# Kernel optimization log

Measured on AMD Instinct MI355X. Metric: run time of the kernel, lower is better.

Reference implementation:

```python
import jax, jax.numpy as jnp
import numpy as np

NEG_SLOPE = 0.2  # PyG GATConv default negative_slope


def gat_conv(x, src, dst, W, a_src, a_dst, b, concat):
    """One PyG-style GATConv (eval mode, self-loops already added to src/dst).
    x: [N, Fin], W: [Fin, H*C], a_src/a_dst: [H, C], b: [H*C] or [C].
    """
    N = x.shape[0]
    H, C = a_src.shape
    h = (x @ W).reshape(N, H, C)                       # [N,H,C]
    alpha_s = jnp.sum(h * a_src, axis=-1)              # [N,H]
    alpha_d = jnp.sum(h * a_dst, axis=-1)              # [N,H]
    e = alpha_s[src] + alpha_d[dst]                    # [E,H]
    e = jax.nn.leaky_relu(e, NEG_SLOPE)
    # scatter-softmax over incoming edges of each destination node
    m = jax.ops.segment_max(e, dst, num_segments=N)    # [N,H]
    p = jnp.exp(e - m[dst])                            # [E,H]
    s = jax.ops.segment_sum(p, dst, num_segments=N)    # [N,H]
    alpha = p / s[dst]                                 # [E,H]
    msg = h[src] * alpha[:, :, None]                   # [E,H,C]
    out = jax.ops.segment_sum(msg, dst, num_segments=N)  # [N,H,C]
    out = out.reshape(N, H * C) if concat else out.mean(axis=1)
    return out + b


def setup_inputs() -> dict:
    key = jax.random.key(0)
    ks = jax.random.split(key, 12)
    N, E = 50000, 800000
    IN_C, HID, HEADS, OUT_C = 1, 32, 4, 1
    HW = HID * HEADS  # 128
    x = jax.random.normal(ks[0], (N, IN_C), dtype=jnp.float32)
    edge_index = jax.random.randint(ks[1], (2, E), 0, N, dtype=jnp.int64)
    g = 0.1
    inp = {
        "x": x,
        "edge_index": edge_index,
        "W1": jax.random.normal(ks[2], (IN_C, HW), dtype=jnp.float32) * g,
        "a_src1": jax.random.normal(ks[3], (HEADS, HID), dtype=jnp.float32) * g,
        "a_dst1": jax.random.normal(ks[4], (HEADS, HID), dtype=jnp.float32) * g,
        "b1": jnp.zeros((HW,), dtype=jnp.float32),
        "W2": jax.random.normal(ks[5], (HW, HW), dtype=jnp.float32) * g,
        "a_src2": jax.random.normal(ks[6], (HEADS, HID), dtype=jnp.float32) * g,
        "a_dst2": jax.random.normal(ks[7], (HEADS, HID), dtype=jnp.float32) * g,
        "b2": jnp.zeros((HW,), dtype=jnp.float32),
        "W3": jax.random.normal(ks[8], (HW, OUT_C), dtype=jnp.float32) * g,
        "a_src3": jax.random.normal(ks[9], (1, OUT_C), dtype=jnp.float32) * g,
        "a_dst3": jax.random.normal(ks[10], (1, OUT_C), dtype=jnp.float32) * g,
        "b3": jnp.zeros((OUT_C,), dtype=jnp.float32),
    }
    return inp


def reference(x, edge_index, W1, a_src1, a_dst1, b1, W2, a_src2, a_dst2, b2,
              W3, a_src3, a_dst3, b3):
    N = x.shape[0]
    loop = jnp.arange(N, dtype=edge_index.dtype)
    # PyG GATConv add_self_loops=True (each layer): add once, reused by all layers
    src = jnp.concatenate([edge_index[0], loop])
    dst = jnp.concatenate([edge_index[1], loop])
    h = gat_conv(x, src, dst, W1, a_src1, a_dst1, b1, concat=True)
    h = jax.nn.elu(h)  # dropout is identity in eval mode
    h = gat_conv(h, src, dst, W2, a_src2, a_dst2, b2, concat=True)
    h = jax.nn.elu(h)
    out = gat_conv(h, src, dst, W3, a_src3, a_dst3, b3, concat=False)
    return out
```

## Files before the change

kernel.cpp:

```cpp
#include <hip/hip_runtime.h>
#include <math.h>

#define NEG_SLOPE 0.2f
#define MAXDEG 64

typedef _Float16 hv4 __attribute__((ext_vector_type(4)));
typedef _Float16 hv8 __attribute__((ext_vector_type(8)));
typedef unsigned short usv4 __attribute__((ext_vector_type(4)));

static __device__ __forceinline__ float leaky(float v){ return v > 0.f ? v : NEG_SLOPE * v; }
static __device__ __forceinline__ float eluf(float v){ return v > 0.f ? v : expm1f(v); }
static __device__ __forceinline__ float eluf_fast(float v){ return v > 0.f ? v : __expf(v) - 1.f; }

__global__ void __launch_bounds__(256) scatter_k(const int* __restrict__ esrc, const int* __restrict__ edst,
                                                 int* __restrict__ cnt, unsigned short* __restrict__ csr,
                                                 int Eg, int Etot, int N){
  const int slot = blockIdx.x & 7;
  const int lo = (int)(((long long)slot * N) >> 3);
  const int hi = (int)(((long long)(slot + 1) * N) >> 3);
  const int stride = (gridDim.x >> 3) * blockDim.x;
  for (int e = (blockIdx.x >> 3) * blockDim.x + threadIdx.x; e < Etot; e += stride){
    int s, d;
    if (e < Eg){ d = edst[e]; if (d < lo || d >= hi) continue; s = esrc[e]; }
    else { s = d = e - Eg; if (d < lo || d >= hi) continue; }
    int pos = atomicAdd(&cnt[d], 1);
    if (pos < MAXDEG) csr[((size_t)d << 6) + pos] = (unsigned short)s;
  }
}

__global__ void __launch_bounds__(256) gemm2_k(const int* __restrict__ cnt, const unsigned short* __restrict__ csr,
                                               const float* __restrict__ x,
                                               const float* __restrict__ as1, const float* __restrict__ ad1,
                                               const float* __restrict__ W1f, const float* __restrict__ b1f,
                                               const float* __restrict__ W,
                                               const float* __restrict__ a_s, const float* __restrict__ a_d,
                                               _Float16* __restrict__ hh, float* __restrict__ as_, float* __restrict__ ad_,
                                               int N){
  __shared__ float sA[128][68];
  __shared__ _Float16 sW[2][16][128];
  __shared__ float sR[64][4];
  __shared__ float sDot[8];
  const int t = threadIdx.x;
  const int n0 = blockIdx.x * 64;
  const int tx = t & 15, ty = t >> 4;
  const int c0 = tx * 8, r0 = ty * 4;

  if (t < 128){
    float ps = W1f[t] * as1[t];
    float pd = W1f[t] * ad1[t];
    #pragma unroll
    for (int off = 16; off; off >>= 1){
      ps += __shfl_xor(ps, off, 32);
      pd += __shfl_xor(pd, off, 32);
    }
    if ((t & 31) == 0){ sDot[t >> 5] = ps; sDot[4 + (t >> 5)] = pd; }
  }
  __syncthreads();

  {
    const int nl2 = t >> 2, q = t & 3;
    const int gn = n0 + nl2;
    if (gn < N){
      const float xd = x[gn];
      const float dA0 = sDot[0], dA1 = sDot[1], dA2 = sDot[2], dA3 = sDot[3];
      const float e0d = xd * sDot[4], e1d = xd * sDot[5], e2d = xd * sDot[6], e3d = xd * sDot[7];
      const int start = gn << 6;
      int dg = cnt[gn]; dg = dg < MAXDEG ? dg : MAXDEG;
      const int endi = start + dg;
      float s0 = 0.f, s1 = 0.f, s2 = 0.f, s3 = 0.f;
      float t0 = 0.f, t1 = 0.f, t2 = 0.f, t3 = 0.f;
      int i = start + q;
      if (i < endi){
        int idx = csr[i];
        while (true){
          const int inext = i + 4;
          const bool more = inext < endi;
          const int idxn = csr[more ? inext : i];
          float xs = x[idx];
          float p0 = __expf(leaky(xs * dA0 + e0d));
          float p1 = __expf(leaky(xs * dA1 + e1d));
          float p2 = __expf(leaky(xs * dA2 + e2d));
          float p3 = __expf(leaky(xs * dA3 + e3d));
          s0 += p0; s1 += p1; s2 += p2; s3 += p3;
          t0 += p0 * xs; t1 += p1 * xs; t2 += p2 * xs; t3 += p3 * xs;
          if (!more) break;
          idx = idxn; i = inext;
        }
      }
      #pragma unroll
      for (int off = 2; off; off >>= 1){
        s0 += __shfl_xor(s0, off, 4); t0 += __shfl_xor(t0, off, 4);
        s1 += __shfl_xor(s1, off, 4); t1 += __shfl_xor(t1, off, 4);
        s2 += __shfl_xor(s2, off, 4); t2 += __shfl_xor(t2, off, 4);
        s3 += __shfl_xor(s3, off, 4); t3 += __shfl_xor(t3, off, 4);
      }
      float sq = (q == 0) ? s0 : (q == 1) ? s1 : (q == 2) ? s2 : s3;
      float tq = (q == 0) ? t0 : (q == 1) ? t1 : (q == 2) ? t2 : t3;
      sR[nl2][q] = tq / sq;
    }
  }
  __syncthreads();

  const int wk = t >> 5;
  const int wq = t & 31;

  float4 rw0, rw1;
  auto gloadW = [&](int k0){
    rw0 = *(const float4*)&W[(size_t)(k0 + wk) * 128 + wq * 4];
    rw1 = *(const float4*)&W[(size_t)(k0 + wk + 8) * 128 + wq * 4];
  };
  auto sstoreW = [&](int buf){
    hv4 a = {(_Float16)rw0.x, (_Float16)rw0.y, (_Float16)rw0.z, (_Float16)rw0.w};
    hv4 b = {(_Float16)rw1.x, (_Float16)rw1.y, (_Float16)rw1.z, (_Float16)rw1.w};
    *(hv4*)&sW[buf][wk][wq * 4]     = a;
    *(hv4*)&sW[buf][wk + 8][wq * 4] = b;
  };

  {
    const int nl = t & 63, q = t >> 6;
    const int gn = n0 + nl;
    const bool valid = (gn < N);
    float r = valid ? sR[nl][q] : 0.f;
    #pragma unroll
    for (int j = 0; j < 32; ++j){
      const int c = q * 32 + j;
      float v = W1f[c] * r + b1f[c];
      v = eluf_fast(v);
      sA[c][nl] = valid ? v : 0.f;
    }
  }

  float acc[4][8];
  #pragma unroll
  for (int r = 0; r < 4; ++r)
    #pragma unroll
    for (int c = 0; c < 8; ++c) acc[r][c] = 0.f;

  gloadW(0); sstoreW(0); __syncthreads();

  #pragma unroll 1
  for (int tile = 0; tile < 8; ++tile){
    const int buf = tile & 1;
    if (tile < 7) gloadW((tile + 1) * 16);
    #pragma unroll
    for (int k = 0; k < 16; ++k){
      float4 aa = *(const float4*)&sA[tile * 16 + k][r0];
      hv8 wh = *(const hv8*)&sW[buf][k][c0];
      float av[4] = {aa.x, aa.y, aa.z, aa.w};
      float wv[8];
      #pragma unroll
      for (int c = 0; c < 8; ++c) wv[c] = (float)wh[c];
      #pragma unroll
      for (int r = 0; r < 4; ++r)
        #pragma unroll
        for (int c = 0; c < 8; ++c) acc[r][c] += av[r] * wv[c];
    }
    if (tile < 7){ sstoreW(1 - buf); __syncthreads(); }
  }

  float asv[8], adv[8];
  #pragma unroll
  for (int c = 0; c < 8; ++c){ asv[c] = a_s[c0 + c]; adv[c] = a_d[c0 + c]; }

  const int hd  = tx >> 2;
  const int off = (tx & 3) * 8;

  #pragma unroll
  for (int r = 0; r < 4; ++r){
    int n = n0 + r0 + r;
    if (n >= N) continue;
    hv8 hv;
    #pragma unroll
    for (int c = 0; c < 8; ++c) hv[c] = (_Float16)acc[r][c];
    *(hv8*)&hh[((size_t)hd * N + n) * 32 + off] = hv;
    float ps = 0.f, pd = 0.f;
    #pragma unroll
    for (int c = 0; c < 8; ++c){ ps += acc[r][c] * asv[c]; pd += acc[r][c] * adv[c]; }
    ps += __shfl_xor(ps, 1); ps += __shfl_xor(ps, 2);
    pd += __shfl_xor(pd, 1); pd += __shfl_xor(pd, 2);
    if ((tx & 3) == 0){
      as_[(size_t)hd * N + n] = ps;
      ad_[(size_t)hd * N + n] = pd;
    }
  }
}

__global__ void __launch_bounds__(256) node_aggr2_k(const int* __restrict__ cnt, const unsigned short* __restrict__ csr,
                                                    const float* __restrict__ as_, const float* __restrict__ ad_,
                                                    const _Float16* __restrict__ hh, const float* __restrict__ b2,
                                                    const float* __restrict__ W3, float* __restrict__ h3, int N){
  const int slot   = blockIdx.x & 7;
  const int chunk  = blockIdx.x >> 3;
  const int head   = slot >> 1;
  const int parity = slot & 1;
  const int t  = threadIdx.x;
  const int nl = t >> 2;
  const int q  = t & 3;
  const int base = chunk * 256 + parity * 128 + nl;
  const float* __restrict__ ash = as_ + (size_t)head * N;
  const _Float16* __restrict__ hhh = hh + (size_t)head * N * 32 + q * 8;
  const int c0 = head * 32 + q * 8;

  #pragma unroll 1
  for (int half = 0; half < 2; ++half){
    const int node = base + half * 64;
    if (node >= N) continue;
    const int start = node << 6;
    int dg = cnt[node]; dg = dg < MAXDEG ? dg : MAXDEG;
    const int end = start + dg;
    const float adv = ad_[(size_t)head * N + node];

    float s = 0.f;
    float acc[8] = {0.f, 0.f, 0.f, 0.f, 0.f, 0.f, 0.f, 0.f};
    int i = start;

    const int iend4 = start + (dg & ~3);
    if (i < iend4){
      usv4 ia = *(const usv4*)&csr[i];
      while (i < iend4){
        const int inext = i + 4;
        const int ipf = (inext < iend4) ? inext : i;
        usv4 ib = *(const usv4*)&csr[ipf];
        const int sx = ia.x, sy = ia.y, sz = ia.z, sw = ia.w;
        const int mysrc = (q == 0) ? sx : (q == 1) ? sy : (q == 2) ? sz : sw;
        float aq = ash[mysrc];
        hv8 h0 = *(const hv8*)&hhh[(size_t)sx * 32];
        hv8 h1 = *(const hv8*)&hhh[(size_t)sy * 32];
        hv8 h2 = *(const hv8*)&hhh[(size_t)sz * 32];
        hv8 h3v = *(const hv8*)&hhh[(size_t)sw * 32];
        float pq = __expf(leaky(aq + adv));
        float p0 = __shfl(pq, 0, 4);
        float p1 = __shfl(pq, 1, 4);
        float p2 = __shfl(pq, 2, 4);
        float p3 = __shfl(pq, 3, 4);
        s += (p0 + p1) + (p2 + p3);
        #pragma unroll
        for (int c = 0; c < 8; ++c)
          acc[c] += (float)h0[c]*p0 + (float)h1[c]*p1 + (float)h2[c]*p2 + (float)h3v[c]*p3;
        ia = ib; i = inext;
      }
    }
    for (; i < end; ++i){
      int src = csr[i];
      float p = __expf(leaky(ash[src] + adv));
      hv8 hv = *(const hv8*)&hhh[(size_t)src * 32];
      s += p;
      #pragma unroll
      for (int c = 0; c < 8; ++c) acc[c] += (float)hv[c] * p;
    }

    const float inv = 1.f / s;
    float part = 0.f;
    #pragma unroll
    for (int c = 0; c < 8; ++c){
      float v = eluf_fast(acc[c] * inv + b2[c0 + c]);
      part += v * W3[c0 + c];
    }
    part += __shfl_xor(part, 1, 4);
    part += __shfl_xor(part, 2, 4);
    if (q == 0) unsafeAtomicAdd(&h3[node], part);
  }
}

__global__ void __launch_bounds__(256) node_aggr3_k(const int* __restrict__ cnt, const unsigned short* __restrict__ csr,
                                                    const float* __restrict__ h3,
                                                    const float* __restrict__ a_s3, const float* __restrict__ a_d3,
                                                    const float* __restrict__ b3,
                                                    float* __restrict__ out, int N){
  int node = blockIdx.x * 32 + (threadIdx.x >> 3);
  if (node >= N) return;
  int q = threadIdx.x & 7;
  const int start = node << 6;
  int dg = cnt[node]; dg = dg < MAXDEG ? dg : MAXDEG;
  const int end = start + dg;
  const float a_s3v = a_s3[0];
  const float adv = a_d3[0] * h3[node];
  float s = 0.f, acc = 0.f;
  int i = start + q;
  if (i < end){
    int idx = csr[i];
    while (true){
      const int inext = i + 8;
      const bool more = inext < end;
      const int idxn = csr[more ? inext : i];
      float hv = h3[idx];
      float p = __expf(leaky(a_s3v * hv + adv));
      s += p; acc += hv * p;
      if (!more) break;
      idx = idxn; i = inext;
    }
  }
  #pragma unroll
  for (int off = 4; off; off >>= 1){
    s += __shfl_xor(s, off, 8);
    acc += __shfl_xor(acc, off, 8);
  }
  if (q == 0) out[node] = acc / s + b3[0];
}

extern "C" void kernel_launch(void* const* d_in, const int* in_sizes, int n_in,
                              void* d_out, int out_size, void* d_ws, size_t ws_size,
                              hipStream_t stream){
  const float* x   = (const float*)d_in[0];
  const int*   ei  = (const int*)  d_in[1];
  const float* W1  = (const float*)d_in[2];
  const float* as1 = (const float*)d_in[3];
  const float* ad1 = (const float*)d_in[4];
  const float* b1  = (const float*)d_in[5];
  const float* W2  = (const float*)d_in[6];
  const float* as2 = (const float*)d_in[7];
  const float* ad2 = (const float*)d_in[8];
  const float* b2  = (const float*)d_in[9];
  const float* W3  = (const float*)d_in[10];
  const float* as3 = (const float*)d_in[11];
  const float* ad3 = (const float*)d_in[12];
  const float* b3  = (const float*)d_in[13];

  const int N    = in_sizes[0];
  const int Eg   = in_sizes[1] / 2;
  const int Etot = Eg + N;
  const int* esrc = ei;
  const int* edst = ei + Eg;

  char* w = (char*)d_ws;
  auto carve = [&](size_t bytes)->char*{
    char* p = w; w += (bytes + 15) & ~size_t(15); return p;
  };
  _Float16* hbuf = (_Float16*)carve((size_t)N * 128 * 2);
  float* asb    = (float*)carve((size_t)N * 4 * 4);
  float* adb    = (float*)carve((size_t)N * 4 * 4);
  float* h3b    = (float*)carve((size_t)N * 4);
  int*   cnt    = (int*)  carve((size_t)N * 4);
  unsigned short* csr16 = (unsigned short*)carve((size_t)N * MAXDEG * 2);

  const int B = 256;
  auto cdiv = [](int a, int b){ return (a + b - 1) / b; };

  hipMemsetAsync(cnt, 0, (size_t)N * 4, stream);
  hipMemsetAsync(h3b, 0, (size_t)N * 4, stream);
  scatter_k<<<128 * 8, B, 0, stream>>>(esrc, edst, cnt, csr16, Eg, Etot, N);

  gemm2_k<<<cdiv(N, 64), B, 0, stream>>>(cnt, csr16, x, as1, ad1, W1, b1,
                                         W2, as2, ad2, hbuf, asb, adb, N);
  node_aggr2_k<<<cdiv(N, 256) * 8, B, 0, stream>>>(cnt, csr16, asb, adb,
                                                   hbuf, b2, W3, h3b, N);

  node_aggr3_k<<<cdiv(N, 32), B, 0, stream>>>(cnt, csr16, h3b, as3, ad3, b3, (float*)d_out, N);
}
```

Baseline: 229.4 us.

## Use packed fp16 dot2 in layer-2 GEMM with fully staged weights

```diff
diff --git a/kernel.cpp b/kernel.cpp
--- a/kernel.cpp
+++ b/kernel.cpp
@@ -4,7 +4,7 @@
 #define NEG_SLOPE 0.2f
 #define MAXDEG 64
 
-typedef _Float16 hv4 __attribute__((ext_vector_type(4)));
+typedef _Float16 hv2 __attribute__((ext_vector_type(2)));
 typedef _Float16 hv8 __attribute__((ext_vector_type(8)));
 typedef unsigned short usv4 __attribute__((ext_vector_type(4)));
 
@@ -36,8 +36,8 @@
                                                const float* __restrict__ a_s, const float* __restrict__ a_d,
                                                _Float16* __restrict__ hh, float* __restrict__ as_, float* __restrict__ ad_,
                                                int N){
-  __shared__ float sA[128][68];
-  __shared__ _Float16 sW[2][16][128];
+  __shared__ hv2 sAh[64][68];
+  __shared__ hv2 sWh[64][128];
   __shared__ float sR[64][4];
   __shared__ float sDot[8];
   const int t = threadIdx.x;
@@ -56,6 +56,21 @@
     if ((t & 31) == 0){ sDot[t >> 5] = ps; sDot[4 + (t >> 5)] = pd; }
   }
   __syncthreads();
+
+  {
+    const int pk0 = t >> 5;
+    const int wq  = t & 31;
+    #pragma unroll 1
+    for (int pass = 0; pass < 8; ++pass){
+      const int pk = pass * 8 + pk0;
+      float4 rw0 = *(const float4*)&W[(size_t)(2 * pk)     * 128 + wq * 4];
+      float4 rw1 = *(const float4*)&W[(size_t)(2 * pk + 1) * 128 + wq * 4];
+      sWh[pk][wq * 4 + 0] = hv2{(_Float16)rw0.x, (_Float16)rw1.x};
+      sWh[pk][wq * 4 + 1] = hv2{(_Float16)rw0.y, (_Float16)rw1.y};
+      sWh[pk][wq * 4 + 2] = hv2{(_Float16)rw0.z, (_Float16)rw1.z};
+      sWh[pk][wq * 4 + 3] = hv2{(_Float16)rw0.w, (_Float16)rw1.w};
+    }
+  }
 
   {
     const int nl2 = t >> 2, q = t & 3;
@@ -101,32 +116,17 @@
   }
   __syncthreads();
 
-  const int wk = t >> 5;
-  const int wq = t & 31;
-
-  float4 rw0, rw1;
-  auto gloadW = [&](int k0){
-    rw0 = *(const float4*)&W[(size_t)(k0 + wk) * 128 + wq * 4];
-    rw1 = *(const float4*)&W[(size_t)(k0 + wk + 8) * 128 + wq * 4];
-  };
-  auto sstoreW = [&](int buf){
-    hv4 a = {(_Float16)rw0.x, (_Float16)rw0.y, (_Float16)rw0.z, (_Float16)rw0.w};
-    hv4 b = {(_Float16)rw1.x, (_Float16)rw1.y, (_Float16)rw1.z, (_Float16)rw1.w};
-    *(hv4*)&sW[buf][wk][wq * 4]     = a;
-    *(hv4*)&sW[buf][wk + 8][wq * 4] = b;
-  };
-
   {
     const int nl = t & 63, q = t >> 6;
     const int gn = n0 + nl;
     const bool valid = (gn < N);
     float r = valid ? sR[nl][q] : 0.f;
     #pragma unroll
-    for (int j = 0; j < 32; ++j){
-      const int c = q * 32 + j;
-      float v = W1f[c] * r + b1f[c];
-      v = eluf_fast(v);
-      sA[c][nl] = valid ? v : 0.f;
+    for (int j = 0; j < 16; ++j){
+      const int c = q * 32 + 2 * j;
+      float v0 = eluf_fast(W1f[c]     * r + b1f[c]);
+      float v1 = eluf_fast(W1f[c + 1] * r + b1f[c + 1]);
+      sAh[c >> 1][nl] = valid ? hv2{(_Float16)v0, (_Float16)v1} : hv2{(_Float16)0.f, (_Float16)0.f};
     }
   }
 
@@ -136,26 +136,29 @@
     #pragma unroll
     for (int c = 0; c < 8; ++c) acc[r][c] = 0.f;
 
-  gloadW(0); sstoreW(0); __syncthreads();
+  __syncthreads();
 
   #pragma unroll 1
   for (int tile = 0; tile < 8; ++tile){
-    const int buf = tile & 1;
-    if (tile < 7) gloadW((tile + 1) * 16);
-    #pragma unroll
-    for (int k = 0; k < 16; ++k){
-      float4 aa = *(const float4*)&sA[tile * 16 + k][r0];
-      hv8 wh = *(const hv8*)&sW[buf][k][c0];
-      float av[4] = {aa.x, aa.y, aa.z, aa.w};
-      float wv[8];
-      #pragma unroll
-      for (int c = 0; c < 8; ++c) wv[c] = (float)wh[c];
+    #pragma unroll
+    for (int k8 = 0; k8 < 8; ++k8){
+      const int kp = tile * 8 + k8;
+      hv8 av = *(const hv8*)&sAh[kp][r0];
+      hv8 wv0 = *(const hv8*)&sWh[kp][c0];
+      hv8 wv1 = *(const hv8*)&sWh[kp][c0 + 4];
+      hv2 a[4], w[8];
+      #pragma unroll
+      for (int r = 0; r < 4; ++r) a[r] = hv2{av[2*r], av[2*r+1]};
+      #pragma unroll
+      for (int c = 0; c < 4; ++c) w[c] = hv2{wv0[2*c], wv0[2*c+1]};
+      #pragma unroll
+      for (int c = 0; c < 4; ++c) w[4+c] = hv2{wv1[2*c], wv1[2*c+1]};
       #pragma unroll
       for (int r = 0; r < 4; ++r)
         #pragma unroll
-        for (int c = 0; c < 8; ++c) acc[r][c] += av[r] * wv[c];
-    }
-    if (tile < 7){ sstoreW(1 - buf); __syncthreads(); }
+        for (int c = 0; c < 8; ++c)
+          acc[r][c] = __builtin_amdgcn_fdot2(a[r], w[c], acc[r][c], false);
+    }
   }
 
   float asv[8], adv[8];
```

Result: faster. 220.9 us (median of 2 runs) (-3.7%).
